# Kernel optimization log

Measured on AMD Instinct MI355X. Metric: run time of the kernel, lower is better.

## Reference

```python
import jax, jax.numpy as jnp
import numpy as np

N = 100000
E = 800000
D_IN = 256
D_H = 512


def setup_inputs() -> dict:
    key = jax.random.key(0)
    ks = jax.random.split(key, 8)
    s_in = 1.0 / np.sqrt(D_IN)
    s_h = 1.0 / np.sqrt(D_H)
    return {
        "x": jax.random.normal(ks[0], (N, D_IN), jnp.float32),
        "edge_index": jax.random.randint(ks[1], (2, E), 0, N, dtype=jnp.int64),
        "W1": jax.random.normal(ks[2], (D_IN, D_H), jnp.float32) * s_in,
        "b1": jnp.zeros((D_H,), jnp.float32),
        "W2": jax.random.normal(ks[3], (D_H, D_H), jnp.float32) * s_h,
        "b2": jnp.zeros((D_H,), jnp.float32),
        "W3": jax.random.normal(ks[4], (D_H, D_H), jnp.float32) * s_h,
        "b3": jnp.zeros((D_H,), jnp.float32),
        "Wfc": jax.random.normal(ks[5], (D_H, D_IN), jnp.float32) * s_h,
        "bfc": jnp.zeros((D_IN,), jnp.float32),
    }


def _gcn_prep(edge_index, n_nodes):
    # PyG GCNConv: add self-loops, symmetric deg^{-1/2} normalization.
    loop = jnp.arange(n_nodes, dtype=edge_index.dtype)
    row = jnp.concatenate([edge_index[0], loop])  # destination
    col = jnp.concatenate([edge_index[1], loop])  # source
    deg = jax.ops.segment_sum(jnp.ones_like(row, dtype=jnp.float32), row,
                              num_segments=n_nodes)
    dinv = jax.lax.rsqrt(deg)  # deg >= 1 due to self loops
    norm = dinv[row] * dinv[col]  # [E+N]
    return row, col, norm


def _gcn_conv(x, W, b, row, col, norm, n_nodes):
    h = x @ W  # [N, out]
    msg = h[col] * norm[:, None]  # [E+N, out] gather + scale
    out = jax.ops.segment_sum(msg, row, num_segments=n_nodes)  # scatter-add
    return out + b


def reference(x, edge_index, W1, b1, W2, b2, W3, b3, Wfc, bfc):
    n = x.shape[0]
    row, col, norm = _gcn_prep(edge_index, n)
    h = jax.nn.relu(_gcn_conv(x, W1, b1, row, col, norm, n))
    h = jax.nn.relu(_gcn_conv(h, W2, b2, row, col, norm, n))
    h = jax.nn.relu(_gcn_conv(h, W3, b3, row, col, norm, n))
    return h @ Wfc + bfc
```

## Files before the change

### kernel.cpp

```cpp
#include <hip/hip_runtime.h>

#define N_NODES 100000
#define NPAD    100096
#define E_EDGES 800000

typedef _Float16 f16;
typedef _Float16 f16x4 __attribute__((ext_vector_type(4)));
typedef _Float16 f16x8 __attribute__((ext_vector_type(8)));
typedef float    f32x4 __attribute__((ext_vector_type(4)));

__device__ inline void async16(const void* g, void* l) {
    __builtin_amdgcn_global_load_lds(
        (const __attribute__((address_space(1))) void*)g,
        (__attribute__((address_space(3))) void*)l, 16, 0, 0);
}

__global__ void k_deg(const int* __restrict__ ei, int* __restrict__ deg) {
    int e = blockIdx.x * 256 + threadIdx.x;
    if (e < E_EDGES) atomicAdd(&deg[ei[e]], 1);
}

__global__ void k_scan1(const int* __restrict__ deg, int* __restrict__ off,
                        int* __restrict__ bsum, float* __restrict__ dinv) {
    __shared__ int s[256];
    int i = blockIdx.x * 256 + threadIdx.x;
    int v = (i < N_NODES) ? deg[i] : 0;
    if (i < N_NODES) dinv[i] = rsqrtf((float)(v + 1));
    s[threadIdx.x] = v;
    __syncthreads();
    for (int d = 1; d < 256; d <<= 1) {
        int t = (threadIdx.x >= d) ? s[threadIdx.x - d] : 0;
        __syncthreads();
        s[threadIdx.x] += t;
        __syncthreads();
    }
    if (i < N_NODES) off[i] = s[threadIdx.x] - v;
    if (threadIdx.x == 255) bsum[blockIdx.x] = s[255];
}

__global__ void k_scan2(int* __restrict__ bsum, int nb) {
    __shared__ int s[512];
    int tid = threadIdx.x;
    int v = (tid < nb) ? bsum[tid] : 0;
    s[tid] = v;
    __syncthreads();
    for (int d = 1; d < 512; d <<= 1) {
        int t = (tid >= d) ? s[tid - d] : 0;
        __syncthreads();
        s[tid] += t;
        __syncthreads();
    }
    if (tid < nb) bsum[tid] = s[tid] - v;
}

__global__ void k_scan3(int* __restrict__ off, const int* __restrict__ bsum) {
    int i = blockIdx.x * 256 + threadIdx.x;
    if (i < N_NODES) off[i] += bsum[blockIdx.x];
    if (i == 0) off[N_NODES] = E_EDGES;
}

__global__ void k_fill(const int* __restrict__ ei, const int* __restrict__ off,
                       int* __restrict__ cursor, int* __restrict__ csr) {
    int e = blockIdx.x * 256 + threadIdx.x;
    if (e >= E_EDGES) return;
    int dst = ei[e];
    int src = ei[E_EDGES + e];
    int pos = atomicAdd(&cursor[dst], 1);
    csr[off[dst] + pos] = src;
}

__global__ void k_x_to_f16(const float* __restrict__ x, f16* __restrict__ xh) {
    int i = blockIdx.x * 256 + threadIdx.x;
    if (i >= (N_NODES * 256) / 4) return;
    float4 v = ((const float4*)x)[i];
    f16x4 o;
    o.x = (f16)v.x; o.y = (f16)v.y; o.z = (f16)v.z; o.w = (f16)v.w;
    ((f16x4*)xh)[i] = o;
}

__global__ void k_transpose(const float* __restrict__ W, f16* __restrict__ Wt,
                            int K, int M) {
    int m = blockIdx.x * 256 + threadIdx.x;
    int k = blockIdx.y;
    if (m < M) Wt[(size_t)m * K + k] = (f16)W[(size_t)k * M + m];
}

template<int K, int M, int MODE>
__launch_bounds__(256, 2)
__global__ void k_gemm(const f16* __restrict__ A, const f16* __restrict__ B,
                       void* __restrict__ C, const float* __restrict__ bias) {
    __shared__ f16 As[128 * 32];
    __shared__ f16 Bs[128 * 32];
    int tid  = threadIdx.x;
    int wave = tid >> 6, lane = tid & 63;
    int wr = (wave >> 1) * 64, wc = (wave & 1) * 64;
    int lm = lane & 15, q = lane >> 4;
    int rowBase = blockIdx.x * 128;
    int colBase = blockIdx.y * 128;

    f32x4 acc[4][4] = {};
    const f16* Ag = A + (size_t)rowBase * K;
    const f16* Bg = B + (size_t)colBase * K;

    int c0 = tid, c1 = tid + 256;
    for (int kt = 0; kt < K; kt += 32) {
        __syncthreads();
        async16(Ag + (size_t)(c0 >> 2) * K + kt + (c0 & 3) * 8, &As[c0 * 8]);
        async16(Ag + (size_t)(c1 >> 2) * K + kt + (c1 & 3) * 8, &As[c1 * 8]);
        async16(Bg + (size_t)(c0 >> 2) * K + kt + (c0 & 3) * 8, &Bs[c0 * 8]);
        async16(Bg + (size_t)(c1 >> 2) * K + kt + (c1 & 3) * 8, &Bs[c1 * 8]);
        __syncthreads();

        f16x8 a[4], b[4];
#pragma unroll
        for (int i = 0; i < 4; ++i) {
            a[i] = *(const f16x8*)&As[(wr + i * 16 + lm) * 32 + q * 8];
            b[i] = *(const f16x8*)&Bs[(wc + i * 16 + lm) * 32 + q * 8];
        }
#pragma unroll
        for (int i = 0; i < 4; ++i)
#pragma unroll
            for (int j = 0; j < 4; ++j)
                acc[i][j] = __builtin_amdgcn_mfma_f32_16x16x32_f16(
                    a[i], b[j], acc[i][j], 0, 0, 0);
    }

#pragma unroll
    for (int i = 0; i < 4; ++i) {
        int gr0 = rowBase + wr + i * 16 + q * 4;
#pragma unroll
        for (int j = 0; j < 4; ++j) {
            int gc = colBase + wc + j * 16 + lm;
#pragma unroll
            for (int r = 0; r < 4; ++r) {
                int gr = gr0 + r;
                if (gr < N_NODES) {
                    float v = acc[i][j][r];
                    if (MODE == 2) {
                        ((float*)C)[(size_t)gr * M + gc] = v + bias[gc];
                    } else if (MODE == 1) {
                        float rr = v + bias[gc];
                        ((f16*)C)[(size_t)gr * M + gc] = (f16)(rr > 0.f ? rr : 0.f);
                    } else {
                        ((f16*)C)[(size_t)gr * M + gc] = (f16)v;
                    }
                }
            }
        }
    }
}

template<int VE> struct VecT;
template<> struct VecT<4> { typedef f16x4 type; };
template<> struct VecT<8> { typedef f16x8 type; };

template<int CH, bool ACT>
__global__ void k_agg(const f16* __restrict__ t, const int* __restrict__ off,
                      const int* __restrict__ csr, const float* __restrict__ dinv,
                      const float* __restrict__ bias, f16* __restrict__ h) {
    constexpr int VE = CH / 64;
    typedef typename VecT<VE>::type vec;
    int node = blockIdx.x * 4 + (threadIdx.x >> 6);
    if (node >= N_NODES) return;
    int lane = threadIdx.x & 63;
    float di = dinv[node];

    const vec* rows = (const vec*)t;
    vec v = rows[(size_t)node * 64 + lane];
    float acc[VE];
#pragma unroll
    for (int j = 0; j < VE; ++j) acc[j] = di * (float)v[j];

    int s = off[node], e = off[node + 1];
    int idx = s;
    for (; idx + 4 <= e; idx += 4) {
        int i0 = csr[idx], i1 = csr[idx + 1], i2 = csr[idx + 2], i3 = csr[idx + 3];
        vec u0 = rows[(size_t)i0 * 64 + lane];
        vec u1 = rows[(size_t)i1 * 64 + lane];
        vec u2 = rows[(size_t)i2 * 64 + lane];
        vec u3 = rows[(size_t)i3 * 64 + lane];
        float d0 = dinv[i0], d1 = dinv[i1], d2 = dinv[i2], d3 = dinv[i3];
#pragma unroll
        for (int j = 0; j < VE; ++j)
            acc[j] += d0 * (float)u0[j] + d1 * (float)u1[j]
                    + d2 * (float)u2[j] + d3 * (float)u3[j];
    }
    for (; idx < e; ++idx) {
        int src = csr[idx];
        float dj = dinv[src];
        vec u = rows[(size_t)src * 64 + lane];
#pragma unroll
        for (int j = 0; j < VE; ++j) acc[j] += dj * (float)u[j];
    }

    vec o;
#pragma unroll
    for (int j = 0; j < VE; ++j) {
        float r = di * acc[j];
        if (ACT) {
            r += bias[lane * VE + j];
            r = r > 0.f ? r : 0.f;
        }
        o[j] = (f16)r;
    }
    ((vec*)h)[(size_t)node * 64 + lane] = o;
}

extern "C" void kernel_launch(void* const* d_in, const int* in_sizes, int n_in,
                              void* d_out, int out_size, void* d_ws, size_t ws_size,
                              hipStream_t stream) {
    const float* x   = (const float*)d_in[0];
    const int*   ei  = (const int*)d_in[1];
    const float* W1  = (const float*)d_in[2];
    const float* b1  = (const float*)d_in[3];
    const float* W2  = (const float*)d_in[4];
    const float* b2  = (const float*)d_in[5];
    const float* W3  = (const float*)d_in[6];
    const float* b3  = (const float*)d_in[7];
    const float* Wfc = (const float*)d_in[8];
    const float* bfc = (const float*)d_in[9];

    char* wsb = (char*)d_ws;
    size_t o = 0;
    auto alloc = [&](size_t bytes) -> void* {
        void* p = wsb + o;
        o += (bytes + 255) & ~(size_t)255;
        return p;
    };

    f16* xh   = (f16*)alloc((size_t)NPAD * 256 * 2);
    f16* t    = (f16*)alloc((size_t)NPAD * 512 * 2);
    f16* h    = (f16*)alloc((size_t)NPAD * 512 * 2);
    f16* Wt1  = (f16*)alloc(512 * 256 * 2);
    f16* Wt2  = (f16*)alloc(512 * 512 * 2);
    f16* Wt3  = (f16*)alloc(512 * 512 * 2);
    f16* Wtfc = (f16*)alloc(256 * 512 * 2);
    int* deg    = (int*)alloc(N_NODES * 4);
    float* dinv = (float*)alloc(N_NODES * 4);
    int* off    = (int*)alloc((N_NODES + 1) * 4);
    int* cursor = (int*)alloc(N_NODES * 4);
    int* bsum   = (int*)alloc(4096 * 4);
    int* csr    = (int*)alloc((size_t)E_EDGES * 4);

    f16* a1 = t;

    const int NB = (N_NODES + 255) / 256;

    hipMemsetAsync(deg, 0, N_NODES * 4, stream);
    hipMemsetAsync(cursor, 0, N_NODES * 4, stream);

    k_deg<<<(E_EDGES + 255) / 256, 256, 0, stream>>>(ei, deg);
    k_scan1<<<NB, 256, 0, stream>>>(deg, off, bsum, dinv);
    k_scan2<<<1, 512, 0, stream>>>(bsum, NB);
    k_scan3<<<NB, 256, 0, stream>>>(off, bsum);
    k_fill<<<(E_EDGES + 255) / 256, 256, 0, stream>>>(ei, off, cursor, csr);

    k_x_to_f16<<<(N_NODES * 256 / 4 + 255) / 256, 256, 0, stream>>>(x, xh);
    k_transpose<<<dim3(2, 256), 256, 0, stream>>>(W1, Wt1, 256, 512);
    k_transpose<<<dim3(2, 512), 256, 0, stream>>>(W2, Wt2, 512, 512);
    k_transpose<<<dim3(2, 512), 256, 0, stream>>>(W3, Wt3, 512, 512);
    k_transpose<<<dim3(1, 512), 256, 0, stream>>>(Wfc, Wtfc, 512, 256);

    dim3 g4(NPAD / 128, 4), g2(NPAD / 128, 2);
    const int AGG_GRID = N_NODES / 4;

    k_agg<256, false><<<AGG_GRID, 256, 0, stream>>>(xh, off, csr, dinv, nullptr, a1);
    k_gemm<256, 512, 1><<<g4, 256, 0, stream>>>(a1, Wt1, h, b1);
    k_gemm<512, 512, 0><<<g4, 256, 0, stream>>>(h, Wt2, t, nullptr);
    k_agg<512, true><<<AGG_GRID, 256, 0, stream>>>(t, off, csr, dinv, b2, h);
    k_gemm<512, 512, 0><<<g4, 256, 0, stream>>>(h, Wt3, t, nullptr);
    k_agg<512, true><<<AGG_GRID, 256, 0, stream>>>(t, off, csr, dinv, b3, h);
    k_gemm<512, 256, 2><<<g2, 256, 0, stream>>>(h, Wtfc, d_out, bfc);
}
```

Before: 942.5 us.

## Split GEMM output into column halves and stage epilogue stores via LDS

The GEMM epilogue now writes each wave's accumulators to shared memory, then issues 16-byte vector stores instead of scattered 2-byte stores. For the hidden layers it writes the output as two 256-column half matrices, so the aggregation kernel can run a 2-D grid where each block gathers only one half. This shrinks the gathered working set per pass, which should improve cache locality, and the new aggregation unrolls neighbour gathers four at a time. The cost is extra block barriers in the epilogue and a second grid dimension that reads the CSR twice.

```diff
diff --git a/kernel.cpp b/kernel.cpp
--- a/kernel.cpp
+++ b/kernel.cpp
@@ -3,6 +3,7 @@
 #define N_NODES 100000
 #define NPAD    100096
 #define E_EDGES 800000
+#define HALF_STRIDE ((size_t)NPAD * 256)
 
 typedef _Float16 f16;
 typedef _Float16 f16x4 __attribute__((ext_vector_type(4)));
@@ -85,12 +86,13 @@
     if (m < M) Wt[(size_t)m * K + k] = (f16)W[(size_t)k * M + m];
 }
 
-template<int K, int M, int MODE>
+template<int K, int M, int MODE, bool SPLIT>
 __launch_bounds__(256, 2)
 __global__ void k_gemm(const f16* __restrict__ A, const f16* __restrict__ B,
                        void* __restrict__ C, const float* __restrict__ bias) {
-    __shared__ f16 As[128 * 32];
-    __shared__ f16 Bs[128 * 32];
+    __shared__ __align__(16) char smem[16384];
+    f16* As = (f16*)smem;
+    f16* Bs = (f16*)(smem + 8192);
     int tid  = threadIdx.x;
     int wave = tid >> 6, lane = tid & 63;
     int wr = (wave >> 1) * 64, wc = (wave & 1) * 64;
@@ -125,27 +127,56 @@
                     a[i], b[j], acc[i][j], 0, 0, 0);
     }
 
-#pragma unroll
-    for (int i = 0; i < 4; ++i) {
-        int gr0 = rowBase + wr + i * 16 + q * 4;
-#pragma unroll
-        for (int j = 0; j < 4; ++j) {
-            int gc = colBase + wc + j * 16 + lm;
-#pragma unroll
-            for (int r = 0; r < 4; ++r) {
-                int gr = gr0 + r;
-                if (gr < N_NODES) {
-                    float v = acc[i][j][r];
-                    if (MODE == 2) {
-                        ((float*)C)[(size_t)gr * M + gc] = v + bias[gc];
-                    } else if (MODE == 1) {
-                        float rr = v + bias[gc];
-                        ((f16*)C)[(size_t)gr * M + gc] = (f16)(rr > 0.f ? rr : 0.f);
-                    } else {
-                        ((f16*)C)[(size_t)gr * M + gc] = (f16)v;
-                    }
+    if (MODE == 2) {
+#pragma unroll
+        for (int i = 0; i < 4; ++i) {
+            int gr0 = rowBase + wr + i * 16 + q * 4;
+#pragma unroll
+            for (int j = 0; j < 4; ++j) {
+                int gc = colBase + wc + j * 16 + lm;
+                float bj = bias[gc];
+#pragma unroll
+                for (int r = 0; r < 4; ++r) {
+                    int gr = gr0 + r;
+                    if (gr < N_NODES)
+                        ((float*)C)[(size_t)gr * M + gc] = acc[i][j][r] + bj;
                 }
             }
+        }
+    } else {
+        __syncthreads();
+        f16* Ep = (f16*)smem + wave * (16 * 80);
+#pragma unroll
+        for (int i = 0; i < 4; ++i) {
+#pragma unroll
+            for (int j = 0; j < 4; ++j) {
+                int colg = colBase + wc + j * 16 + lm;
+#pragma unroll
+                for (int r = 0; r < 4; ++r) {
+                    float v = acc[i][j][r];
+                    if (MODE == 1) {
+                        v += bias[colg];
+                        v = v > 0.f ? v : 0.f;
+                    }
+                    Ep[(q * 4 + r) * 80 + j * 16 + lm] = (f16)v;
+                }
+            }
+            __syncthreads();
+            int row0 = lane >> 3, c8 = lane & 7;
+            f16x8 v0 = *(const f16x8*)&Ep[row0 * 80 + c8 * 8];
+            f16x8 v1 = *(const f16x8*)&Ep[(row0 + 8) * 80 + c8 * 8];
+            int gr0 = rowBase + wr + i * 16 + row0;
+            int gc  = colBase + wc + c8 * 8;
+            if (SPLIT) {
+                f16* base = (f16*)C + (size_t)(gc >> 8) * HALF_STRIDE;
+                int cl = gc & 255;
+                *(f16x8*)&base[(size_t)gr0 * 256 + cl] = v0;
+                *(f16x8*)&base[(size_t)(gr0 + 8) * 256 + cl] = v1;
+            } else {
+                *(f16x8*)&((f16*)C)[(size_t)gr0 * M + gc] = v0;
+                *(f16x8*)&((f16*)C)[(size_t)(gr0 + 8) * M + gc] = v1;
+            }
+            __syncthreads();
         }
     }
 }
@@ -204,6 +235,57 @@
         o[j] = (f16)r;
     }
     ((vec*)h)[(size_t)node * 64 + lane] = o;
+}
+
+template<bool ACT>
+__global__ void k_agg_split(const f16* __restrict__ t, const int* __restrict__ off,
+                            const int* __restrict__ csr, const float* __restrict__ dinv,
+                            const float* __restrict__ bias, f16* __restrict__ h) {
+    int node = blockIdx.x * 4 + (threadIdx.x >> 6);
+    if (node >= N_NODES) return;
+    int half = blockIdx.y;
+    int lane = threadIdx.x & 63;
+    float di = dinv[node];
+
+    const f16x4* rows = (const f16x4*)(t + (size_t)half * HALF_STRIDE);
+    f16x4 v = rows[(size_t)node * 64 + lane];
+    float acc[4];
+#pragma unroll
+    for (int j = 0; j < 4; ++j) acc[j] = di * (float)v[j];
+
+    int s = off[node], e = off[node + 1];
+    int idx = s;
+    for (; idx + 4 <= e; idx += 4) {
+        int i0 = csr[idx], i1 = csr[idx + 1], i2 = csr[idx + 2], i3 = csr[idx + 3];
+        f16x4 u0 = rows[(size_t)i0 * 64 + lane];
+        f16x4 u1 = rows[(size_t)i1 * 64 + lane];
+        f16x4 u2 = rows[(size_t)i2 * 64 + lane];
+        f16x4 u3 = rows[(size_t)i3 * 64 + lane];
+        float d0 = dinv[i0], d1 = dinv[i1], d2 = dinv[i2], d3 = dinv[i3];
+#pragma unroll
+        for (int j = 0; j < 4; ++j)
+            acc[j] += d0 * (float)u0[j] + d1 * (float)u1[j]
+                    + d2 * (float)u2[j] + d3 * (float)u3[j];
+    }
+    for (; idx < e; ++idx) {
+        int src = csr[idx];
+        float dj = dinv[src];
+        f16x4 u = rows[(size_t)src * 64 + lane];
+#pragma unroll
+        for (int j = 0; j < 4; ++j) acc[j] += dj * (float)u[j];
+    }
+
+    f16x4 o;
+#pragma unroll
+    for (int j = 0; j < 4; ++j) {
+        float r = di * acc[j];
+        if (ACT) {
+            r += bias[half * 256 + lane * 4 + j];
+            r = r > 0.f ? r : 0.f;
+        }
+        o[j] = (f16)r;
+    }
+    *(f16x4*)&h[(size_t)node * 512 + half * 256 + lane * 4] = o;
 }
 
 extern "C" void kernel_launch(void* const* d_in, const int* in_sizes, int n_in,
@@ -263,12 +345,13 @@
 
     dim3 g4(NPAD / 128, 4), g2(NPAD / 128, 2);
     const int AGG_GRID = N_NODES / 4;
+    dim3 gs(AGG_GRID, 2);
 
     k_agg<256, false><<<AGG_GRID, 256, 0, stream>>>(xh, off, csr, dinv, nullptr, a1);
-    k_gemm<256, 512, 1><<<g4, 256, 0, stream>>>(a1, Wt1, h, b1);
-    k_gemm<512, 512, 0><<<g4, 256, 0, stream>>>(h, Wt2, t, nullptr);
-    k_agg<512, true><<<AGG_GRID, 256, 0, stream>>>(t, off, csr, dinv, b2, h);
-    k_gemm<512, 512, 0><<<g4, 256, 0, stream>>>(h, Wt3, t, nullptr);
-    k_agg<512, true><<<AGG_GRID, 256, 0, stream>>>(t, off, csr, dinv, b3, h);
-    k_gemm<512, 256, 2><<<g2, 256, 0, stream>>>(h, Wtfc, d_out, bfc);
-}
+    k_gemm<256, 512, 1, false><<<g4, 256, 0, stream>>>(a1, Wt1, h, b1);
+    k_gemm<512, 512, 0, true><<<g4, 256, 0, stream>>>(h, Wt2, t, nullptr);
+    k_agg_split<true><<<gs, 256, 0, stream>>>(t, off, csr, dinv, b2, h);
+    k_gemm<512, 512, 0, true><<<g4, 256, 0, stream>>>(h, Wt3, t, nullptr);
+    k_agg_split<true><<<gs, 256, 0, stream>>>(t, off, csr, dinv, b3, h);
+    k_gemm<512, 256, 2, false><<<g2, 256, 0, stream>>>(h, Wtfc, d_out, bfc);
+}
```

New measurement: 922.3 us. -2.1%, faster.
